# Kernel optimization log

Measured on AMD Instinct MI355X. Metric: run time of the kernel, lower is better.

The kernel has to match this reference:

```python
import jax, jax.numpy as jnp
import numpy as np

EPS = 1e-12  # torch F.normalize eps
ALPHA = 100.0


def _l2norm(v, axis):
    n = jnp.sqrt(jnp.sum(v * v, axis=axis, keepdims=True))
    return v / jnp.maximum(n, EPS)


def setup_inputs() -> dict:
    key = jax.random.key(0)
    kx, kc = jax.random.split(key)
    B, D, H, W, K = 16, 512, 64, 64, 64
    x = jax.random.normal(kx, (B, D, H, W), dtype=jnp.float32)
    centroids = jax.random.uniform(kc, (K, D), dtype=jnp.float32)
    # NetVLAD._init_params: conv weight/bias derived from centroids at init
    conv_w = 2.0 * ALPHA * centroids                 # [K, D] (1x1 conv kernel)
    conv_b = -ALPHA * jnp.linalg.norm(centroids, axis=1)  # [K]
    return {"x": x, "centroids": centroids, "conv_w": conv_w, "conv_b": conv_b}


def reference(x, centroids, conv_w, conv_b):
    B, D = x.shape[:2]
    K = centroids.shape[0]
    # descriptor-wise L2 normalization over channel dim
    x = _l2norm(x, axis=1)
    xf = x.reshape(B, D, -1)                          # [B, D, N]
    # 1x1 conv == per-position matmul: [B, K, N]
    logits = jnp.einsum('kd,bdn->bkn', conv_w, xf) + conv_b[None, :, None]
    assign = jax.nn.softmax(logits, axis=1)           # soft assignment over K
    # vlad[b,k,d] = sum_n a[b,k,n]*(x[b,d,n] - c[k,d])
    #            = (a @ x^T) - a.sum(n) * c   (avoids B*K*D*N intermediate)
    agg = jnp.einsum('bkn,bdn->bkd', assign, xf)      # [B, K, D]
    mass = jnp.sum(assign, axis=-1)                   # [B, K]
    vlad = agg - mass[..., None] * centroids[None]    # [B, K, D]
    vlad = _l2norm(vlad, axis=2)                      # intra-normalization
    vlad = vlad.reshape(B, -1)                        # [B, K*D]
    return _l2norm(vlad, axis=1)
```

## Files before the change

kernel.cpp:

```cpp
#include <hip/hip_runtime.h>
#include <cstddef>

constexpr int Bn = 16, Dn = 512, Nn = 4096, Kn = 64;
constexpr int PN = 128;
constexpr int Dp = 520;
constexpr float FEPS = 1e-12f;

typedef __bf16 bf16x8 __attribute__((ext_vector_type(8)));
typedef float f32x4 __attribute__((ext_vector_type(4)));

__device__ __forceinline__ unsigned short bf_bits(__bf16 h) {
  union { __bf16 b; unsigned short u; } c;
  c.b = h;
  return c.u;
}

__global__ __launch_bounds__(256) void kW(const float* __restrict__ w,
                                          unsigned short* __restrict__ w_hi,
                                          unsigned short* __restrict__ w_lo) {
  const int idx = blockIdx.x * 256 + threadIdx.x;
  const float v = w[idx];
  const __bf16 h = (__bf16)v;
  const float r = v - (float)h;
  const __bf16 l = (__bf16)r;
  w_hi[idx] = bf_bits(h);
  w_lo[idx] = bf_bits(l);
}

__global__ __launch_bounds__(512, 2) void kF(const float* __restrict__ x,
                                             const unsigned short* __restrict__ w_hi,
                                             const unsigned short* __restrict__ w_lo,
                                             const float* __restrict__ conv_b,
                                             float* __restrict__ aggp,
                                             float* __restrict__ massp) {
  __shared__ float xs[PN * 33];
  __shared__ unsigned short xhi[Dn * PN];
  __shared__ float msum[8][64];
  const int tid = threadIdx.x;
  const int l = tid & 63;
  const int wv = tid >> 6;
  const int ll = l & 15;
  const int lg = l >> 4;
  const int b = blockIdx.x >> 4;
  const int sp = blockIdx.x & 15;
  const int srow = tid >> 4;
  const int sc0 = (tid & 15) << 3;
  const int ncol = (wv << 4) + ll;

  f32x4 acc2[4][4];
#pragma unroll
  for (int kt = 0; kt < 4; ++kt)
#pragma unroll
    for (int dt = 0; dt < 4; ++dt) acc2[kt][dt] = (f32x4){0.f, 0.f, 0.f, 0.f};

  for (int rep = 0; rep < 2; ++rep) {
    const int p = (sp << 1) + rep;
    const int n0 = p << 7;
    const float* xbp = x + (size_t)b * Dn * Nn + n0;

    f32x4 acc[4];
#pragma unroll
    for (int kt = 0; kt < 4; ++kt) acc[kt] = (f32x4){0.f, 0.f, 0.f, 0.f};
    float ss = 0.f;

    float4 pf0 = *(const float4*)(xbp + (size_t)srow * Nn + sc0);
    float4 pf1 = *(const float4*)(xbp + (size_t)srow * Nn + sc0 + 4);

    for (int dc = 0; dc < Dn; dc += 32) {
      const float pv[8] = {pf0.x, pf0.y, pf0.z, pf0.w, pf1.x, pf1.y, pf1.z, pf1.w};
#pragma unroll
      for (int j = 0; j < 8; ++j) xs[(sc0 + j) * 33 + srow] = pv[j];
      {
        unsigned short hb[8];
#pragma unroll
        for (int j = 0; j < 8; ++j) hb[j] = bf_bits((__bf16)pv[j]);
        const unsigned byteoff =
            (unsigned)(((dc + srow) * PN + sc0) * 2) ^ ((unsigned)(srow & 7) << 4);
        uint4 hv;
        hv.x = (unsigned)hb[0] | ((unsigned)hb[1] << 16);
        hv.y = (unsigned)hb[2] | ((unsigned)hb[3] << 16);
        hv.z = (unsigned)hb[4] | ((unsigned)hb[5] << 16);
        hv.w = (unsigned)hb[6] | ((unsigned)hb[7] << 16);
        *(uint4*)((char*)xhi + byteoff) = hv;
      }
      if (dc + 32 < Dn) {
        pf0 = *(const float4*)(xbp + (size_t)(dc + 32 + srow) * Nn + sc0);
        pf1 = *(const float4*)(xbp + (size_t)(dc + 32 + srow) * Nn + sc0 + 4);
      }
      asm volatile("s_waitcnt lgkmcnt(0)\ns_barrier" ::: "memory");

      float xv[8];
#pragma unroll
      for (int j = 0; j < 8; ++j) xv[j] = xs[ncol * 33 + lg * 8 + j];
      bf16x8 bh, bl;
#pragma unroll
      for (int j = 0; j < 8; ++j) {
        ss = fmaf(xv[j], xv[j], ss);
        const __bf16 h = (__bf16)xv[j];
        bh[j] = h;
        bl[j] = (__bf16)(xv[j] - (float)h);
      }
#pragma unroll
      for (int kt = 0; kt < 4; ++kt) {
        const size_t woff = (size_t)(kt * 16 + ll) * Dn + dc + lg * 8;
        bf16x8 ah = *(const bf16x8*)(w_hi + woff);
        bf16x8 al = *(const bf16x8*)(w_lo + woff);
        acc[kt] = __builtin_amdgcn_mfma_f32_16x16x32_bf16(ah, bh, acc[kt], 0, 0, 0);
        acc[kt] = __builtin_amdgcn_mfma_f32_16x16x32_bf16(ah, bl, acc[kt], 0, 0, 0);
        acc[kt] = __builtin_amdgcn_mfma_f32_16x16x32_bf16(al, bh, acc[kt], 0, 0, 0);
      }
      asm volatile("s_waitcnt lgkmcnt(0)\ns_barrier" ::: "memory");
    }

    ss += __shfl_xor(ss, 16);
    ss += __shfl_xor(ss, 32);
    const float iv = 1.f / fmaxf(sqrtf(ss), FEPS);
    float lgt[16];
#pragma unroll
    for (int kt = 0; kt < 4; ++kt)
#pragma unroll
      for (int r = 0; r < 4; ++r)
        lgt[kt * 4 + r] = fmaf(acc[kt][r], iv, conv_b[kt * 16 + lg * 4 + r]);
    float pmax = lgt[0];
#pragma unroll
    for (int i = 1; i < 16; ++i) pmax = fmaxf(pmax, lgt[i]);
    pmax = fmaxf(pmax, __shfl_xor(pmax, 16));
    pmax = fmaxf(pmax, __shfl_xor(pmax, 32));
    float ex[16];
    float psum = 0.f;
#pragma unroll
    for (int i = 0; i < 16; ++i) {
      ex[i] = expf(lgt[i] - pmax);
      psum += ex[i];
    }
    psum += __shfl_xor(psum, 16);
    psum += __shfl_xor(psum, 32);
    const float isum = 1.f / psum;

    __syncthreads();

    unsigned short* as_hi = (unsigned short*)xs;
    const int ngb = (wv << 1) + (ll >> 3);
    const int jj = ll & 7;
#pragma unroll
    for (int i = 0; i < 16; ++i) {
      const int k = (i >> 2) * 16 + lg * 4 + (i & 3);
      const float a = ex[i] * isum;
      as_hi[(ngb * 64 + k) * 8 + jj] = bf_bits((__bf16)(a * iv));
      float m = a;
      m += __shfl_xor(m, 1);
      m += __shfl_xor(m, 2);
      m += __shfl_xor(m, 4);
      m += __shfl_xor(m, 8);
      if (ll == 0) msum[wv][k] = m;
    }
    __syncthreads();
    if (tid < 64) {
      float s = 0.f;
#pragma unroll
      for (int ww = 0; ww < 8; ++ww) s += msum[ww][tid];
      massp[((b << 5) + p) * Kn + tid] = s;
    }

#pragma unroll
    for (int nc = 0; nc < PN; nc += 32) {
      const int ng = (nc >> 3) + lg;
      bf16x8 af[4];
#pragma unroll
      for (int kt = 0; kt < 4; ++kt)
        af[kt] = *(const bf16x8*)(as_hi + (ng * 64 + kt * 16 + ll) * 8);
#pragma unroll
      for (int dt = 0; dt < 4; ++dt) {
        const int d = wv * 64 + dt * 16 + ll;
        const unsigned byteoff =
            (unsigned)((d * PN + nc + lg * 8) * 2) ^ ((unsigned)(d & 7) << 4);
        bf16x8 bx = *(const bf16x8*)((const char*)xhi + byteoff);
#pragma unroll
        for (int kt = 0; kt < 4; ++kt)
          acc2[kt][dt] = __builtin_amdgcn_mfma_f32_16x16x32_bf16(
              af[kt], bx, acc2[kt][dt], 0, 0, 0);
      }
    }
    __syncthreads();
  }

  float* outb = aggp + (size_t)((b << 4) + sp) * Kn * Dp;
#pragma unroll
  for (int kt = 0; kt < 4; ++kt)
#pragma unroll
    for (int dt = 0; dt < 4; ++dt) {
      const int krow = kt * 16 + (lg << 2);
      const int dcol = wv * 64 + dt * 16 + ll;
      float* op = outb + (size_t)krow * Dp + dcol;
#pragma unroll
      for (int r = 0; r < 4; ++r) op[(size_t)r * Dp] = acc2[kt][dt][r];
    }
}

__device__ __forceinline__ float blockReduceSum(float v, float* sb) {
#pragma unroll
  for (int off = 32; off > 0; off >>= 1) v += __shfl_down(v, off, 64);
  const int lane = threadIdx.x & 63, w = threadIdx.x >> 6;
  if (lane == 0) sb[w] = v;
  __syncthreads();
  if (threadIdx.x == 0) sb[4] = sb[0] + sb[1] + sb[2] + sb[3];
  __syncthreads();
  return sb[4];
}

__global__ __launch_bounds__(256) void kC1(const float* __restrict__ massp,
                                           const float* __restrict__ aggp,
                                           const float* __restrict__ centroids,
                                           float* __restrict__ out,
                                           float* __restrict__ rowsq) {
  __shared__ float sb[5];
  const int tid = threadIdx.x;
  const int b = blockIdx.x >> 6, k = blockIdx.x & 63;
  float s = 0.f;
  if (tid < 32) s = massp[((b << 5) + tid) * Kn + k];
  const float mass = blockReduceSum(s, sb);
  float v[2];
  float sq = 0.f;
#pragma unroll
  for (int u = 0; u < 2; ++u) {
    const int d = tid + (u << 8);
    float val = -mass * centroids[k * Dn + d];
#pragma unroll
    for (int pp = 0; pp < 16; ++pp)
      val += aggp[((size_t)((b << 4) + pp) * Kn + k) * Dp + d];
    v[u] = val;
    sq = fmaf(val, val, sq);
  }
  const float rsq = blockReduceSum(sq, sb);
  const float inv = 1.f / fmaxf(sqrtf(rsq), FEPS);
#pragma unroll
  for (int u = 0; u < 2; ++u)
    out[((size_t)b * Kn + k) * Dn + tid + (u << 8)] = v[u] * inv;
  if (tid == 0) rowsq[b * Kn + k] = rsq * inv * inv;
}

__global__ __launch_bounds__(256) void kC2(float* __restrict__ out,
                                           const float* __restrict__ rowsq) {
  __shared__ float sg;
  const int b = blockIdx.x, tid = threadIdx.x;
  float v = (tid < 64) ? rowsq[b * Kn + tid] : 0.f;
  if (tid < 64) {
#pragma unroll
    for (int off = 32; off > 0; off >>= 1) v += __shfl_down(v, off, 64);
  }
  if (tid == 0) sg = 1.f / fmaxf(sqrtf(v), FEPS);
  __syncthreads();
  const float inv = sg;
  float* ob = out + (size_t)b * (Kn * Dn);
  for (int t = tid; t < Kn * Dn; t += 256) ob[t] *= inv;
}

extern "C" void kernel_launch(void* const* d_in, const int* in_sizes, int n_in,
                              void* d_out, int out_size, void* d_ws,
                              size_t ws_size, hipStream_t stream) {
  const float* x = (const float*)d_in[0];
  const float* centroids = (const float*)d_in[1];
  const float* conv_w = (const float*)d_in[2];
  const float* conv_b = (const float*)d_in[3];
  float* out = (float*)d_out;
  float* ws = (float*)d_ws;
  float* aggp = ws;
  unsigned short* w_hi = (unsigned short*)(ws + 8519680);
  unsigned short* w_lo = (unsigned short*)(ws + 8536064);
  float* massp = ws + 8552448;
  float* rowsq = ws + 8585216;

  kW<<<128, 256, 0, stream>>>(conv_w, w_hi, w_lo);
  kF<<<256, 512, 0, stream>>>(x, w_hi, w_lo, conv_b, aggp, massp);
  kC1<<<1024, 256, 0, stream>>>(massp, aggp, centroids, out, rowsq);
  kC2<<<16, 256, 0, stream>>>(out, rowsq);
}
```

Baseline: 123.2 us.

## Split fused kernel to one position tile per block and shrink LDS cache

Each block now handles a single 128-position tile instead of looping over two, doubling the grid to 512 blocks and doubling the partial aggregate buffers that the reduction kernel sums. The bf16 copy of x kept in shared memory is cut to the first 240 channels so that LDS use drops enough to allow four blocks per CU. The remaining channels are re-read from global memory and converted to bf16 in the second matmul. This trades extra global reads and a larger partial-sum reduction for higher occupancy and more parallelism.

```diff
diff --git a/kernel.cpp b/kernel.cpp
--- a/kernel.cpp
+++ b/kernel.cpp
@@ -3,6 +3,7 @@
 
 constexpr int Bn = 16, Dn = 512, Nn = 4096, Kn = 64;
 constexpr int PN = 128;
+constexpr int XHD = 240;
 constexpr int Dp = 520;
 constexpr float FEPS = 1e-12f;
 
@@ -27,25 +28,131 @@
   w_lo[idx] = bf_bits(l);
 }
 
-__global__ __launch_bounds__(512, 2) void kF(const float* __restrict__ x,
+__global__ __launch_bounds__(512, 4) void kF(const float* __restrict__ x,
                                              const unsigned short* __restrict__ w_hi,
                                              const unsigned short* __restrict__ w_lo,
                                              const float* __restrict__ conv_b,
                                              float* __restrict__ aggp,
                                              float* __restrict__ massp) {
   __shared__ float xs[PN * 33];
-  __shared__ unsigned short xhi[Dn * PN];
+  __shared__ unsigned short xhi[XHD * PN];
   __shared__ float msum[8][64];
   const int tid = threadIdx.x;
   const int l = tid & 63;
   const int wv = tid >> 6;
   const int ll = l & 15;
   const int lg = l >> 4;
-  const int b = blockIdx.x >> 4;
-  const int sp = blockIdx.x & 15;
+  const int b = blockIdx.x >> 5;
+  const int p = blockIdx.x & 31;
+  const int n0 = p << 7;
   const int srow = tid >> 4;
   const int sc0 = (tid & 15) << 3;
   const int ncol = (wv << 4) + ll;
+  const float* xbp = x + (size_t)b * Dn * Nn + n0;
+
+  f32x4 acc[4];
+#pragma unroll
+  for (int kt = 0; kt < 4; ++kt) acc[kt] = (f32x4){0.f, 0.f, 0.f, 0.f};
+  float ss = 0.f;
+
+  float4 pf0 = *(const float4*)(xbp + (size_t)srow * Nn + sc0);
+  float4 pf1 = *(const float4*)(xbp + (size_t)srow * Nn + sc0 + 4);
+
+  for (int dc = 0; dc < Dn; dc += 32) {
+    const float pv[8] = {pf0.x, pf0.y, pf0.z, pf0.w, pf1.x, pf1.y, pf1.z, pf1.w};
+#pragma unroll
+    for (int j = 0; j < 8; ++j) xs[(sc0 + j) * 33 + srow] = pv[j];
+    if (dc + srow < XHD) {
+      unsigned short hb[8];
+#pragma unroll
+      for (int j = 0; j < 8; ++j) hb[j] = bf_bits((__bf16)pv[j]);
+      const unsigned byteoff =
+          (unsigned)(((dc + srow) * PN + sc0) * 2) ^ ((unsigned)(srow & 7) << 4);
+      uint4 hv;
+      hv.x = (unsigned)hb[0] | ((unsigned)hb[1] << 16);
+      hv.y = (unsigned)hb[2] | ((unsigned)hb[3] << 16);
+      hv.z = (unsigned)hb[4] | ((unsigned)hb[5] << 16);
+      hv.w = (unsigned)hb[6] | ((unsigned)hb[7] << 16);
+      *(uint4*)((char*)xhi + byteoff) = hv;
+    }
+    if (dc + 32 < Dn) {
+      pf0 = *(const float4*)(xbp + (size_t)(dc + 32 + srow) * Nn + sc0);
+      pf1 = *(const float4*)(xbp + (size_t)(dc + 32 + srow) * Nn + sc0 + 4);
+    }
+    asm volatile("s_waitcnt lgkmcnt(0)\ns_barrier" ::: "memory");
+
+    float xv[8];
+#pragma unroll
+    for (int j = 0; j < 8; ++j) xv[j] = xs[ncol * 33 + lg * 8 + j];
+    bf16x8 bh, bl;
+#pragma unroll
+    for (int j = 0; j < 8; ++j) {
+      ss = fmaf(xv[j], xv[j], ss);
+      const __bf16 h = (__bf16)xv[j];
+      bh[j] = h;
+      bl[j] = (__bf16)(xv[j] - (float)h);
+    }
+#pragma unroll
+    for (int kt = 0; kt < 4; ++kt) {
+      const size_t woff = (size_t)(kt * 16 + ll) * Dn + dc + lg * 8;
+      bf16x8 ah = *(const bf16x8*)(w_hi + woff);
+      bf16x8 al = *(const bf16x8*)(w_lo + woff);
+      acc[kt] = __builtin_amdgcn_mfma_f32_16x16x32_bf16(ah, bh, acc[kt], 0, 0, 0);
+      acc[kt] = __builtin_amdgcn_mfma_f32_16x16x32_bf16(ah, bl, acc[kt], 0, 0, 0);
+      acc[kt] = __builtin_amdgcn_mfma_f32_16x16x32_bf16(al, bh, acc[kt], 0, 0, 0);
+    }
+    asm volatile("s_waitcnt lgkmcnt(0)\ns_barrier" ::: "memory");
+  }
+
+  ss += __shfl_xor(ss, 16);
+  ss += __shfl_xor(ss, 32);
+  const float iv = 1.f / fmaxf(sqrtf(ss), FEPS);
+  float lgt[16];
+#pragma unroll
+  for (int kt = 0; kt < 4; ++kt)
+#pragma unroll
+    for (int r = 0; r < 4; ++r)
+      lgt[kt * 4 + r] = fmaf(acc[kt][r], iv, conv_b[kt * 16 + lg * 4 + r]);
+  float pmax = lgt[0];
+#pragma unroll
+  for (int i = 1; i < 16; ++i) pmax = fmaxf(pmax, lgt[i]);
+  pmax = fmaxf(pmax, __shfl_xor(pmax, 16));
+  pmax = fmaxf(pmax, __shfl_xor(pmax, 32));
+  float ex[16];
+  float psum = 0.f;
+#pragma unroll
+  for (int i = 0; i < 16; ++i) {
+    ex[i] = expf(lgt[i] - pmax);
+    psum += ex[i];
+  }
+  psum += __shfl_xor(psum, 16);
+  psum += __shfl_xor(psum, 32);
+  const float isum = 1.f / psum;
+
+  __syncthreads();
+
+  unsigned short* as_hi = (unsigned short*)xs;
+  const int ngb = (wv << 1) + (ll >> 3);
+  const int jj = ll & 7;
+#pragma unroll
+  for (int i = 0; i < 16; ++i) {
+    const int k = (i >> 2) * 16 + lg * 4 + (i & 3);
+    const float a = ex[i] * isum;
+    as_hi[(ngb * 64 + k) * 8 + jj] = bf_bits((__bf16)(a * iv));
+    float m = a;
+    m += __shfl_xor(m, 1);
+    m += __shfl_xor(m, 2);
+    m += __shfl_xor(m, 4);
+    m += __shfl_xor(m, 8);
+    if (ll == 0) msum[wv][k] = m;
+  }
+  __syncthreads();
+  if (tid < 64) {
+    float s = 0.f;
+#pragma unroll
+    for (int ww = 0; ww < 8; ++ww) s += msum[ww][tid];
+    massp[((b << 5) + p) * Kn + tid] = s;
+  }
 
   f32x4 acc2[4][4];
 #pragma unroll
@@ -53,138 +160,41 @@
 #pragma unroll
     for (int dt = 0; dt < 4; ++dt) acc2[kt][dt] = (f32x4){0.f, 0.f, 0.f, 0.f};
 
-  for (int rep = 0; rep < 2; ++rep) {
-    const int p = (sp << 1) + rep;
-    const int n0 = p << 7;
-    const float* xbp = x + (size_t)b * Dn * Nn + n0;
-
-    f32x4 acc[4];
-#pragma unroll
-    for (int kt = 0; kt < 4; ++kt) acc[kt] = (f32x4){0.f, 0.f, 0.f, 0.f};
-    float ss = 0.f;
-
-    float4 pf0 = *(const float4*)(xbp + (size_t)srow * Nn + sc0);
-    float4 pf1 = *(const float4*)(xbp + (size_t)srow * Nn + sc0 + 4);
-
-    for (int dc = 0; dc < Dn; dc += 32) {
-      const float pv[8] = {pf0.x, pf0.y, pf0.z, pf0.w, pf1.x, pf1.y, pf1.z, pf1.w};
-#pragma unroll
-      for (int j = 0; j < 8; ++j) xs[(sc0 + j) * 33 + srow] = pv[j];
-      {
-        unsigned short hb[8];
-#pragma unroll
-        for (int j = 0; j < 8; ++j) hb[j] = bf_bits((__bf16)pv[j]);
-        const unsigned byteoff =
-            (unsigned)(((dc + srow) * PN + sc0) * 2) ^ ((unsigned)(srow & 7) << 4);
-        uint4 hv;
-        hv.x = (unsigned)hb[0] | ((unsigned)hb[1] << 16);
-        hv.y = (unsigned)hb[2] | ((unsigned)hb[3] << 16);
-        hv.z = (unsigned)hb[4] | ((unsigned)hb[5] << 16);
-        hv.w = (unsigned)hb[6] | ((unsigned)hb[7] << 16);
-        *(uint4*)((char*)xhi + byteoff) = hv;
-      }
-      if (dc + 32 < Dn) {
-        pf0 = *(const float4*)(xbp + (size_t)(dc + 32 + srow) * Nn + sc0);
-        pf1 = *(const float4*)(xbp + (size_t)(dc + 32 + srow) * Nn + sc0 + 4);
-      }
-      asm volatile("s_waitcnt lgkmcnt(0)\ns_barrier" ::: "memory");
-
-      float xv[8];
-#pragma unroll
-      for (int j = 0; j < 8; ++j) xv[j] = xs[ncol * 33 + lg * 8 + j];
-      bf16x8 bh, bl;
-#pragma unroll
-      for (int j = 0; j < 8; ++j) {
-        ss = fmaf(xv[j], xv[j], ss);
-        const __bf16 h = (__bf16)xv[j];
-        bh[j] = h;
-        bl[j] = (__bf16)(xv[j] - (float)h);
-      }
-#pragma unroll
-      for (int kt = 0; kt < 4; ++kt) {
-        const size_t woff = (size_t)(kt * 16 + ll) * Dn + dc + lg * 8;
-        bf16x8 ah = *(const bf16x8*)(w_hi + woff);
-        bf16x8 al = *(const bf16x8*)(w_lo + woff);
-        acc[kt] = __builtin_amdgcn_mfma_f32_16x16x32_bf16(ah, bh, acc[kt], 0, 0, 0);
-        acc[kt] = __builtin_amdgcn_mfma_f32_16x16x32_bf16(ah, bl, acc[kt], 0, 0, 0);
-        acc[kt] = __builtin_amdgcn_mfma_f32_16x16x32_bf16(al, bh, acc[kt], 0, 0, 0);
-      }
-      asm volatile("s_waitcnt lgkmcnt(0)\ns_barrier" ::: "memory");
-    }
-
-    ss += __shfl_xor(ss, 16);
-    ss += __shfl_xor(ss, 32);
-    const float iv = 1.f / fmaxf(sqrtf(ss), FEPS);
-    float lgt[16];
+  const float* xg = x + (size_t)b * Dn * Nn + n0 + lg * 8;
+
+#pragma unroll
+  for (int nc = 0; nc < PN; nc += 32) {
+    const int ng = (nc >> 3) + lg;
+    bf16x8 af[4];
 #pragma unroll
     for (int kt = 0; kt < 4; ++kt)
-#pragma unroll
-      for (int r = 0; r < 4; ++r)
-        lgt[kt * 4 + r] = fmaf(acc[kt][r], iv, conv_b[kt * 16 + lg * 4 + r]);
-    float pmax = lgt[0];
-#pragma unroll
-    for (int i = 1; i < 16; ++i) pmax = fmaxf(pmax, lgt[i]);
-    pmax = fmaxf(pmax, __shfl_xor(pmax, 16));
-    pmax = fmaxf(pmax, __shfl_xor(pmax, 32));
-    float ex[16];
-    float psum = 0.f;
-#pragma unroll
-    for (int i = 0; i < 16; ++i) {
-      ex[i] = expf(lgt[i] - pmax);
-      psum += ex[i];
-    }
-    psum += __shfl_xor(psum, 16);
-    psum += __shfl_xor(psum, 32);
-    const float isum = 1.f / psum;
-
-    __syncthreads();
-
-    unsigned short* as_hi = (unsigned short*)xs;
-    const int ngb = (wv << 1) + (ll >> 3);
-    const int jj = ll & 7;
-#pragma unroll
-    for (int i = 0; i < 16; ++i) {
-      const int k = (i >> 2) * 16 + lg * 4 + (i & 3);
-      const float a = ex[i] * isum;
-      as_hi[(ngb * 64 + k) * 8 + jj] = bf_bits((__bf16)(a * iv));
-      float m = a;
-      m += __shfl_xor(m, 1);
-      m += __shfl_xor(m, 2);
-      m += __shfl_xor(m, 4);
-      m += __shfl_xor(m, 8);
-      if (ll == 0) msum[wv][k] = m;
-    }
-    __syncthreads();
-    if (tid < 64) {
-      float s = 0.f;
-#pragma unroll
-      for (int ww = 0; ww < 8; ++ww) s += msum[ww][tid];
-      massp[((b << 5) + p) * Kn + tid] = s;
-    }
-
-#pragma unroll
-    for (int nc = 0; nc < PN; nc += 32) {
-      const int ng = (nc >> 3) + lg;
-      bf16x8 af[4];
-#pragma unroll
-      for (int kt = 0; kt < 4; ++kt)
-        af[kt] = *(const bf16x8*)(as_hi + (ng * 64 + kt * 16 + ll) * 8);
-#pragma unroll
-      for (int dt = 0; dt < 4; ++dt) {
-        const int d = wv * 64 + dt * 16 + ll;
+      af[kt] = *(const bf16x8*)(as_hi + (ng * 64 + kt * 16 + ll) * 8);
+#pragma unroll
+    for (int dt = 0; dt < 4; ++dt) {
+      const int dbase = wv * 64 + dt * 16;
+      const int d = dbase + ll;
+      bf16x8 bx;
+      if (dbase < XHD) {
         const unsigned byteoff =
             (unsigned)((d * PN + nc + lg * 8) * 2) ^ ((unsigned)(d & 7) << 4);
-        bf16x8 bx = *(const bf16x8*)((const char*)xhi + byteoff);
-#pragma unroll
-        for (int kt = 0; kt < 4; ++kt)
-          acc2[kt][dt] = __builtin_amdgcn_mfma_f32_16x16x32_bf16(
-              af[kt], bx, acc2[kt][dt], 0, 0, 0);
+        bx = *(const bf16x8*)((const char*)xhi + byteoff);
+      } else {
+        const float* xr = xg + (size_t)d * Nn + nc;
+        float4 x0 = *(const float4*)(xr);
+        float4 x1 = *(const float4*)(xr + 4);
+        bx[0] = (__bf16)x0.x; bx[1] = (__bf16)x0.y;
+        bx[2] = (__bf16)x0.z; bx[3] = (__bf16)x0.w;
+        bx[4] = (__bf16)x1.x; bx[5] = (__bf16)x1.y;
+        bx[6] = (__bf16)x1.z; bx[7] = (__bf16)x1.w;
       }
-    }
-    __syncthreads();
-  }
-
-  float* outb = aggp + (size_t)((b << 4) + sp) * Kn * Dp;
+#pragma unroll
+      for (int kt = 0; kt < 4; ++kt)
+        acc2[kt][dt] = __builtin_amdgcn_mfma_f32_16x16x32_bf16(
+            af[kt], bx, acc2[kt][dt], 0, 0, 0);
+    }
+  }
+
+  float* outb = aggp + (size_t)((b << 5) + p) * Kn * Dp;
 #pragma unroll
   for (int kt = 0; kt < 4; ++kt)
 #pragma unroll
@@ -225,9 +235,9 @@
   for (int u = 0; u < 2; ++u) {
     const int d = tid + (u << 8);
     float val = -mass * centroids[k * Dn + d];
-#pragma unroll
-    for (int pp = 0; pp < 16; ++pp)
-      val += aggp[((size_t)((b << 4) + pp) * Kn + k) * Dp + d];
+#pragma unroll 8
+    for (int pp = 0; pp < 32; ++pp)
+      val += aggp[((size_t)((b << 5) + pp) * Kn + k) * Dp + d];
     v[u] = val;
     sq = fmaf(val, val, sq);
   }
@@ -265,13 +275,13 @@
   float* out = (float*)d_out;
   float* ws = (float*)d_ws;
   float* aggp = ws;
-  unsigned short* w_hi = (unsigned short*)(ws + 8519680);
-  unsigned short* w_lo = (unsigned short*)(ws + 8536064);
-  float* massp = ws + 8552448;
-  float* rowsq = ws + 8585216;
+  unsigned short* w_hi = (unsigned short*)(ws + 17039360);
+  unsigned short* w_lo = (unsigned short*)(ws + 17055744);
+  float* massp = ws + 17072128;
+  float* rowsq = ws + 17104896;
 
   kW<<<128, 256, 0, stream>>>(conv_w, w_hi, w_lo);
-  kF<<<256, 512, 0, stream>>>(x, w_hi, w_lo, conv_b, aggp, massp);
+  kF<<<512, 512, 0, stream>>>(x, w_hi, w_lo, conv_b, aggp, massp);
   kC1<<<1024, 256, 0, stream>>>(massp, aggp, centroids, out, rowsq);
   kC2<<<16, 256, 0, stream>>>(out, rowsq);
 }
```

Result: no change. 125.3 us (+1.7%).
